# Kernel tuning notes

Measured on AMD Instinct MI355X. Metric: run time of the kernel, lower is better.

The kernel has to match this reference:

```python
import jax, jax.numpy as jnp
import numpy as np

M, K, N = 8192, 4096, 4096


def setup_inputs() -> dict:
    key = jax.random.key(0)
    k1, k2, k3, k4 = jax.random.split(key, 4)
    x = jax.random.normal(k1, (M, K), dtype=jnp.float32)
    # int8 weight buffer (qweight), per-output-channel dequant scales, bf16-style bias
    weight_q = jax.random.randint(k2, (N, K), -128, 128, dtype=jnp.int32).astype(jnp.int8)
    qscales = jax.random.uniform(k3, (N,), dtype=jnp.float32) * 0.01 + 0.005
    bias = jax.random.normal(k4, (N,), dtype=jnp.float32) * 0.01
    return {"x": x, "weight_q": weight_q, "qscales": qscales, "bias": bias}


def reference(x, weight_q, qscales, bias):
    # dynamic per-tensor activation quantization: clampv = max(x)
    clampv = jnp.max(x)
    x8 = jnp.clip(jnp.round(x * (127.0 / clampv)), -128, 127).astype(jnp.int8)
    acc = jax.lax.dot_general(
        x8, weight_q,
        dimension_numbers=(((1,), (1,)), ((), ())),
        preferred_element_type=jnp.int32,
    )
    # fused dequant: (acc*alpha + bias/qscales)*qscales == acc*alpha*qscales + bias
    out = acc.astype(jnp.float32) * (clampv / 127.0) * qscales[None, :] + bias[None, :]
    return out
```

## Files before the change

### kernel.cpp

```cpp
#include <hip/hip_runtime.h>
#include <math.h>

#define MDIM 8192
#define KDIM 4096
#define NDIM 4096

typedef int v4i __attribute__((ext_vector_type(4)));

__device__ __forceinline__ void gload_lds16(const void* g, void* l) {
  __builtin_amdgcn_global_load_lds(
      (const __attribute__((address_space(1))) void*)g,
      (__attribute__((address_space(3))) void*)l,
      16, 0, 0);
}

__global__ void __launch_bounds__(256) kmax(const float* __restrict__ x,
                                            unsigned int* __restrict__ key_out) {
  const int n4 = MDIM * KDIM / 4;
  int tid = blockIdx.x * blockDim.x + threadIdx.x;
  int stride = gridDim.x * blockDim.x;
  float m = -3.4e38f;
  const float4* x4 = (const float4*)x;
  for (int i = tid; i < n4; i += stride) {
    float4 v = x4[i];
    m = fmaxf(m, fmaxf(fmaxf(v.x, v.y), fmaxf(v.z, v.w)));
  }
  #pragma unroll
  for (int off = 32; off > 0; off >>= 1)
    m = fmaxf(m, __shfl_down(m, off, 64));
  __shared__ float sm[4];
  int lane = threadIdx.x & 63, wv = threadIdx.x >> 6;
  if (lane == 0) sm[wv] = m;
  __syncthreads();
  if (threadIdx.x == 0) {
    m = fmaxf(fmaxf(sm[0], sm[1]), fmaxf(sm[2], sm[3]));
    unsigned b = __float_as_uint(m);
    unsigned key = (b & 0x80000000u) ? ~b : (b | 0x80000000u);
    atomicMax(key_out, key);
  }
}

__device__ __forceinline__ float key_to_float(unsigned key) {
  unsigned b = (key & 0x80000000u) ? (key & 0x7FFFFFFFu) : ~key;
  return __uint_as_float(b);
}

__global__ void __launch_bounds__(256) kdetect(const int* __restrict__ w,
                                               unsigned* __restrict__ mode) {
  int ok = 1;
  #pragma unroll
  for (int i = 0; i < 16; ++i) {
    int v = w[threadIdx.x * 16 + i];
    if (v < -128 || v > 127) ok = 0;
  }
  __shared__ int s;
  if (threadIdx.x == 0) s = 1;
  __syncthreads();
  if (!ok) atomicAnd(&s, 0);
  __syncthreads();
  if (threadIdx.x == 0) *mode = (unsigned)s;
}

__global__ void __launch_bounds__(256) kpackw(const int* __restrict__ w,
                                              signed char* __restrict__ w8,
                                              const unsigned* __restrict__ mode) {
  const int n16 = NDIM * KDIM / 16;
  int tid = blockIdx.x * blockDim.x + threadIdx.x;
  int stride = gridDim.x * blockDim.x;
  int4* dst = (int4*)w8;
  if (*mode) {
    const int4* src = (const int4*)w;
    for (int i = tid; i < n16; i += stride) {
      int4 r;
      #pragma unroll
      for (int q = 0; q < 4; ++q) {
        int4 a = src[(size_t)i * 4 + q];
        int packed = (a.x & 255) | ((a.y & 255) << 8) |
                     ((a.z & 255) << 16) | ((a.w & 255) << 24);
        ((int*)&r)[q] = packed;
      }
      dst[i] = r;
    }
  } else {
    const int4* src = (const int4*)w;
    for (int i = tid; i < n16; i += stride) dst[i] = src[i];
  }
}

__device__ __forceinline__ int pack4(float4 v, float s) {
  int q0 = (int)fminf(fmaxf(rintf(v.x * s), -128.f), 127.f);
  int q1 = (int)fminf(fmaxf(rintf(v.y * s), -128.f), 127.f);
  int q2 = (int)fminf(fmaxf(rintf(v.z * s), -128.f), 127.f);
  int q3 = (int)fminf(fmaxf(rintf(v.w * s), -128.f), 127.f);
  return (q0 & 255) | ((q1 & 255) << 8) | ((q2 & 255) << 16) | ((q3 & 255) << 24);
}

__global__ void __launch_bounds__(256) kquant(const float* __restrict__ x,
                                              signed char* __restrict__ x8,
                                              const unsigned* __restrict__ keyp) {
  float s = 127.0f / key_to_float(*keyp);
  const int n16 = MDIM * KDIM / 16;
  int tid = blockIdx.x * blockDim.x + threadIdx.x;
  int stride = gridDim.x * blockDim.x;
  const float4* x4 = (const float4*)x;
  int4* out16 = (int4*)x8;
  for (int i = tid; i < n16; i += stride) {
    const float4* src = x4 + (size_t)i * 4;
    int4 r;
    r.x = pack4(src[0], s);
    r.y = pack4(src[1], s);
    r.z = pack4(src[2], s);
    r.w = pack4(src[3], s);
    out16[i] = r;
  }
}

constexpr int BM = 256, BN = 256, BK = 128;
constexpr int NT = KDIM / BK;

__device__ __forceinline__ v4i mfma_i8(v4i a, v4i b, v4i c) {
  return __builtin_amdgcn_mfma_i32_16x16x64_i8(a, b, c, 0, 0, 0);
}

__global__ void __launch_bounds__(512, 2) kgemm(
    const signed char* __restrict__ A8,
    const signed char* __restrict__ W8,
    const float* __restrict__ qs,
    const float* __restrict__ bias,
    const unsigned* __restrict__ keyp,
    float* __restrict__ out) {
  __shared__ alignas(1024) signed char lds[2][2][BM * BK];

  const int nbn = NDIM / BN;
  const int nwg = (MDIM / BM) * nbn;
  int bid = blockIdx.x;
  int wg = (bid & 7) * (nwg / 8) + (bid >> 3);
  const int brow = (wg / nbn) * BM;
  const int bcol = (wg % nbn) * BN;

  const int tid = threadIdx.x;
  const int lane = tid & 63;
  const int wv = tid >> 6;
  const int wr = wv >> 2, wc = wv & 3;
  const int lhi = lane >> 4, llo = lane & 15;

  const signed char* Abase = A8 + (size_t)brow * KDIM;
  const signed char* Bbase = W8 + (size_t)bcol * KDIM;

  auto stage = [&](int t) {
    const int buf = t & 1;
    const int k0 = t * BK;
    #pragma unroll
    for (int l = 0; l < 4; ++l) {
      int p = l * 512 + tid;
      int row = p >> 3, slot = p & 7;
      int g = slot ^ (row & 7);
      gload_lds16(Abase + (size_t)row * KDIM + k0 + g * 16, &lds[buf][0][p * 16]);
    }
    #pragma unroll
    for (int l = 0; l < 4; ++l) {
      int p = l * 512 + tid;
      int row = p >> 3, slot = p & 7;
      int g = slot ^ (row & 7);
      gload_lds16(Bbase + (size_t)row * KDIM + k0 + g * 16, &lds[buf][1][p * 16]);
    }
  };

  v4i acc[8][4];
  v4i zero = {0, 0, 0, 0};
  #pragma unroll
  for (int i = 0; i < 8; ++i)
    #pragma unroll
    for (int j = 0; j < 4; ++j) acc[i][j] = zero;

  stage(0);
  stage(1);
  asm volatile("s_waitcnt vmcnt(8)" ::: "memory");
  __builtin_amdgcn_s_barrier();
  __builtin_amdgcn_sched_barrier(0);

  for (int t = 0; t < NT; ++t) {
    const int buf = t & 1;
    const signed char* As = lds[buf][0];
    const signed char* Bs = lds[buf][1];

    v4i bfr[4][2];
    #pragma unroll
    for (int ni = 0; ni < 4; ++ni) {
      int row = wc * 64 + ni * 16 + llo;
      #pragma unroll
      for (int ks = 0; ks < 2; ++ks) {
        int slot = (ks * 4 + lhi) ^ (row & 7);
        bfr[ni][ks] = *(const v4i*)&Bs[row * BK + slot * 16];
      }
    }
    #pragma unroll
    for (int ph = 0; ph < 4; ++ph) {
      v4i afr[2][2];
      #pragma unroll
      for (int i = 0; i < 2; ++i) {
        int row = wr * 128 + (2 * ph + i) * 16 + llo;
        #pragma unroll
        for (int ks = 0; ks < 2; ++ks) {
          int slot = (ks * 4 + lhi) ^ (row & 7);
          afr[i][ks] = *(const v4i*)&As[row * BK + slot * 16];
        }
      }
      __builtin_amdgcn_s_setprio(1);
      #pragma unroll
      for (int ni = 0; ni < 4; ++ni) {
        acc[2 * ph][ni]     = mfma_i8(afr[0][0], bfr[ni][0], acc[2 * ph][ni]);
        acc[2 * ph][ni]     = mfma_i8(afr[0][1], bfr[ni][1], acc[2 * ph][ni]);
        acc[2 * ph + 1][ni] = mfma_i8(afr[1][0], bfr[ni][0], acc[2 * ph + 1][ni]);
        acc[2 * ph + 1][ni] = mfma_i8(afr[1][1], bfr[ni][1], acc[2 * ph + 1][ni]);
      }
      __builtin_amdgcn_s_setprio(0);
    }

    __builtin_amdgcn_s_barrier();
    __builtin_amdgcn_sched_barrier(0);
    if (t + 2 < NT) {
      stage(t + 2);
      asm volatile("s_waitcnt vmcnt(8)" ::: "memory");
    } else {
      asm volatile("s_waitcnt vmcnt(0)" ::: "memory");
    }
    __builtin_amdgcn_s_barrier();
    __builtin_amdgcn_sched_barrier(0);
  }

  const float alpha = key_to_float(*keyp) * (1.0f / 127.0f);
  #pragma unroll
  for (int ni = 0; ni < 4; ++ni) {
    int n = bcol + wc * 64 + ni * 16 + llo;
    float sc = qs[n] * alpha;
    float bv = bias[n];
    #pragma unroll
    for (int mi = 0; mi < 8; ++mi) {
      int m0 = brow + wr * 128 + mi * 16 + lhi * 4;
      #pragma unroll
      for (int j = 0; j < 4; ++j)
        out[(size_t)(m0 + j) * NDIM + n] = (float)acc[mi][ni][j] * sc + bv;
    }
  }
}

extern "C" void kernel_launch(void* const* d_in, const int* in_sizes, int n_in,
                              void* d_out, int out_size, void* d_ws, size_t ws_size,
                              hipStream_t stream) {
  const float* x = (const float*)d_in[0];
  const int* wq = (const int*)d_in[1];
  const float* qscales = (const float*)d_in[2];
  const float* bias = (const float*)d_in[3];
  float* out = (float*)d_out;

  unsigned* keyp = (unsigned*)d_ws;
  unsigned* wmode = (unsigned*)d_ws + 1;
  signed char* x8 = (signed char*)d_ws + 256;
  signed char* w8 = x8 + (size_t)MDIM * KDIM;

  hipMemsetAsync(keyp, 0, 4, stream);
  kdetect<<<1, 256, 0, stream>>>(wq, wmode);
  kpackw<<<2048, 256, 0, stream>>>(wq, w8, wmode);
  kmax<<<2048, 256, 0, stream>>>(x, keyp);
  kquant<<<2048, 256, 0, stream>>>(x, x8, keyp);
  kgemm<<<(MDIM / BM) * (NDIM / BN), 512, 0, stream>>>(x8, w8, qscales, bias, keyp, out);
}
```

Baseline: 231.4 us.

## Split GEMM K-step into four phases with half-tile staged prefetch; fold detect into pack

Restructures the int8 GEMM main loop into four MFMA phases per K-tile. Each phase issues a half-tile async global-to-LDS load for the next tiles and waits with a partial vmcnt, so loads and LDS reads interleave more finely with compute. LDS is split into half-tiles with a remapped row layout, and the loop is unrolled by two. Separately, the weight-format detection kernel is merged into the pack kernel, so every block rechecks the format itself and one launch disappears. This adds more barriers per iteration and relies on vmcnt counts and out-of-range prefetch wrapping (t & (NT-1)) being correct.

New measurement: 223.7 us. 1.03x faster.

```diff
diff --git a/kernel.cpp b/kernel.cpp
--- a/kernel.cpp
+++ b/kernel.cpp
@@ -45,30 +45,26 @@
   return __uint_as_float(b);
 }
 
-__global__ void __launch_bounds__(256) kdetect(const int* __restrict__ w,
-                                               unsigned* __restrict__ mode) {
+__global__ void __launch_bounds__(256) kpackw(const int* __restrict__ w,
+                                              signed char* __restrict__ w8) {
+  __shared__ int smode;
   int ok = 1;
   #pragma unroll
   for (int i = 0; i < 16; ++i) {
     int v = w[threadIdx.x * 16 + i];
-    if (v < -128 || v > 127) ok = 0;
-  }
-  __shared__ int s;
-  if (threadIdx.x == 0) s = 1;
+    ok &= (v >= -128) & (v <= 127);
+  }
+  if (threadIdx.x == 0) smode = 1;
   __syncthreads();
-  if (!ok) atomicAnd(&s, 0);
+  if (!ok) atomicAnd(&smode, 0);
   __syncthreads();
-  if (threadIdx.x == 0) *mode = (unsigned)s;
-}
-
-__global__ void __launch_bounds__(256) kpackw(const int* __restrict__ w,
-                                              signed char* __restrict__ w8,
-                                              const unsigned* __restrict__ mode) {
+  const int mode = smode;
+
   const int n16 = NDIM * KDIM / 16;
   int tid = blockIdx.x * blockDim.x + threadIdx.x;
   int stride = gridDim.x * blockDim.x;
   int4* dst = (int4*)w8;
-  if (*mode) {
+  if (mode) {
     const int4* src = (const int4*)w;
     for (int i = tid; i < n16; i += stride) {
       int4 r;
@@ -122,6 +118,13 @@
   return __builtin_amdgcn_mfma_i32_16x16x64_i8(a, b, c, 0, 0, 0);
 }
 
+#define PHASE_END()                                         \
+  do {                                                      \
+    asm volatile("s_waitcnt vmcnt(10)" ::: "memory");       \
+    __builtin_amdgcn_s_barrier();                           \
+    __builtin_amdgcn_sched_barrier(0);                      \
+  } while (0)
+
 __global__ void __launch_bounds__(512, 2) kgemm(
     const signed char* __restrict__ A8,
     const signed char* __restrict__ W8,
@@ -129,7 +132,7 @@
     const float* __restrict__ bias,
     const unsigned* __restrict__ keyp,
     float* __restrict__ out) {
-  __shared__ alignas(1024) signed char lds[2][2][BM * BK];
+  __shared__ alignas(1024) signed char lds[2][2][2][128 * 128];
 
   const int nbn = NDIM / BN;
   const int nwg = (MDIM / BM) * nbn;
@@ -147,23 +150,41 @@
   const signed char* Abase = A8 + (size_t)brow * KDIM;
   const signed char* Bbase = W8 + (size_t)bcol * KDIM;
 
-  auto stage = [&](int t) {
-    const int buf = t & 1;
-    const int k0 = t * BK;
-    #pragma unroll
-    for (int l = 0; l < 4; ++l) {
+  auto stageA = [&](int t, int h) {
+    signed char* dst = &lds[t & 1][0][h][0];
+    const size_t k0 = (size_t)(t & (NT - 1)) * BK;
+    #pragma unroll
+    for (int l = 0; l < 2; ++l) {
       int p = l * 512 + tid;
-      int row = p >> 3, slot = p & 7;
-      int g = slot ^ (row & 7);
-      gload_lds16(Abase + (size_t)row * KDIM + k0 + g * 16, &lds[buf][0][p * 16]);
-    }
-    #pragma unroll
-    for (int l = 0; l < 4; ++l) {
+      int r = p >> 3, s = p & 7;
+      int R = ((r >> 6) << 7) + h * 64 + (r & 63);
+      int g = s ^ (r & 7);
+      gload_lds16(Abase + (size_t)R * KDIM + k0 + g * 16, dst + p * 16);
+    }
+  };
+  auto stageB = [&](int t, int h) {
+    signed char* dst = &lds[t & 1][1][h][0];
+    const size_t k0 = (size_t)(t & (NT - 1)) * BK;
+    #pragma unroll
+    for (int l = 0; l < 2; ++l) {
       int p = l * 512 + tid;
-      int row = p >> 3, slot = p & 7;
-      int g = slot ^ (row & 7);
-      gload_lds16(Bbase + (size_t)row * KDIM + k0 + g * 16, &lds[buf][1][p * 16]);
-    }
+      int r = p >> 3, s = p & 7;
+      int R = ((r >> 5) << 6) + h * 32 + (r & 31);
+      int g = s ^ (r & 7);
+      gload_lds16(Bbase + (size_t)R * KDIM + k0 + g * 16, dst + p * 16);
+    }
+  };
+  auto readA = [&](int par, int mi, int ks) -> v4i {
+    int h = mi >> 2;
+    int r = wr * 64 + (mi & 3) * 16 + llo;
+    int s = (ks * 4 + lhi) ^ (llo & 7);
+    return *(const v4i*)&lds[par][0][h][r * 128 + s * 16];
+  };
+  auto readB = [&](int par, int ni, int ks) -> v4i {
+    int h = ni >> 1;
+    int r = wc * 32 + (ni & 1) * 16 + llo;
+    int s = (ks * 4 + lhi) ^ (llo & 7);
+    return *(const v4i*)&lds[par][1][h][r * 128 + s * 16];
   };
 
   v4i acc[8][4];
@@ -173,61 +194,95 @@
     #pragma unroll
     for (int j = 0; j < 4; ++j) acc[i][j] = zero;
 
-  stage(0);
-  stage(1);
-  asm volatile("s_waitcnt vmcnt(8)" ::: "memory");
+  stageA(0, 0); stageB(0, 0); stageB(0, 1); stageA(0, 1);
+  stageA(1, 0); stageB(1, 0); stageB(1, 1);
+  asm volatile("s_waitcnt vmcnt(6)" ::: "memory");
   __builtin_amdgcn_s_barrier();
   __builtin_amdgcn_sched_barrier(0);
 
+  #pragma unroll 2
   for (int t = 0; t < NT; ++t) {
-    const int buf = t & 1;
-    const signed char* As = lds[buf][0];
-    const signed char* Bs = lds[buf][1];
-
-    v4i bfr[4][2];
-    #pragma unroll
-    for (int ni = 0; ni < 4; ++ni) {
-      int row = wc * 64 + ni * 16 + llo;
-      #pragma unroll
-      for (int ks = 0; ks < 2; ++ks) {
-        int slot = (ks * 4 + lhi) ^ (row & 7);
-        bfr[ni][ks] = *(const v4i*)&Bs[row * BK + slot * 16];
-      }
-    }
-    #pragma unroll
-    for (int ph = 0; ph < 4; ++ph) {
-      v4i afr[2][2];
-      #pragma unroll
-      for (int i = 0; i < 2; ++i) {
-        int row = wr * 128 + (2 * ph + i) * 16 + llo;
-        #pragma unroll
-        for (int ks = 0; ks < 2; ++ks) {
-          int slot = (ks * 4 + lhi) ^ (row & 7);
-          afr[i][ks] = *(const v4i*)&As[row * BK + slot * 16];
-        }
-      }
-      __builtin_amdgcn_s_setprio(1);
-      #pragma unroll
-      for (int ni = 0; ni < 4; ++ni) {
-        acc[2 * ph][ni]     = mfma_i8(afr[0][0], bfr[ni][0], acc[2 * ph][ni]);
-        acc[2 * ph][ni]     = mfma_i8(afr[0][1], bfr[ni][1], acc[2 * ph][ni]);
-        acc[2 * ph + 1][ni] = mfma_i8(afr[1][0], bfr[ni][0], acc[2 * ph + 1][ni]);
-        acc[2 * ph + 1][ni] = mfma_i8(afr[1][1], bfr[ni][1], acc[2 * ph + 1][ni]);
-      }
-      __builtin_amdgcn_s_setprio(0);
-    }
-
+    const int par = t & 1;
+    v4i afr03[4][2], afr47[4][2], bfr01[2][2], bfr23[2][2];
+
+    #pragma unroll
+    for (int mi = 0; mi < 4; ++mi) {
+      afr03[mi][0] = readA(par, mi, 0);
+      afr03[mi][1] = readA(par, mi, 1);
+    }
+    #pragma unroll
+    for (int ni = 0; ni < 2; ++ni) {
+      bfr01[ni][0] = readB(par, ni, 0);
+      bfr01[ni][1] = readB(par, ni, 1);
+    }
+    stageA(t + 1, 1);
     __builtin_amdgcn_s_barrier();
     __builtin_amdgcn_sched_barrier(0);
-    if (t + 2 < NT) {
-      stage(t + 2);
-      asm volatile("s_waitcnt vmcnt(8)" ::: "memory");
-    } else {
-      asm volatile("s_waitcnt vmcnt(0)" ::: "memory");
-    }
+    __builtin_amdgcn_s_setprio(1);
+    #pragma unroll
+    for (int mi = 0; mi < 4; ++mi)
+      #pragma unroll
+      for (int ni = 0; ni < 2; ++ni) {
+        acc[mi][ni] = mfma_i8(afr03[mi][0], bfr01[ni][0], acc[mi][ni]);
+        acc[mi][ni] = mfma_i8(afr03[mi][1], bfr01[ni][1], acc[mi][ni]);
+      }
+    __builtin_amdgcn_s_setprio(0);
+    PHASE_END();
+
+    #pragma unroll
+    for (int ni = 0; ni < 2; ++ni) {
+      bfr23[ni][0] = readB(par, 2 + ni, 0);
+      bfr23[ni][1] = readB(par, 2 + ni, 1);
+    }
+    stageA(t + 2, 0);
     __builtin_amdgcn_s_barrier();
     __builtin_amdgcn_sched_barrier(0);
-  }
+    __builtin_amdgcn_s_setprio(1);
+    #pragma unroll
+    for (int mi = 0; mi < 4; ++mi)
+      #pragma unroll
+      for (int ni = 0; ni < 2; ++ni) {
+        acc[mi][2 + ni] = mfma_i8(afr03[mi][0], bfr23[ni][0], acc[mi][2 + ni]);
+        acc[mi][2 + ni] = mfma_i8(afr03[mi][1], bfr23[ni][1], acc[mi][2 + ni]);
+      }
+    __builtin_amdgcn_s_setprio(0);
+    PHASE_END();
+
+    #pragma unroll
+    for (int mi = 0; mi < 4; ++mi) {
+      afr47[mi][0] = readA(par, 4 + mi, 0);
+      afr47[mi][1] = readA(par, 4 + mi, 1);
+    }
+    stageB(t + 2, 0);
+    __builtin_amdgcn_s_barrier();
+    __builtin_amdgcn_sched_barrier(0);
+    __builtin_amdgcn_s_setprio(1);
+    #pragma unroll
+    for (int mi = 0; mi < 4; ++mi)
+      #pragma unroll
+      for (int ni = 0; ni < 2; ++ni) {
+        acc[4 + mi][ni] = mfma_i8(afr47[mi][0], bfr01[ni][0], acc[4 + mi][ni]);
+        acc[4 + mi][ni] = mfma_i8(afr47[mi][1], bfr01[ni][1], acc[4 + mi][ni]);
+      }
+    __builtin_amdgcn_s_setprio(0);
+    PHASE_END();
+
+    stageB(t + 2, 1);
+    __builtin_amdgcn_s_barrier();
+    __builtin_amdgcn_sched_barrier(0);
+    __builtin_amdgcn_s_setprio(1);
+    #pragma unroll
+    for (int mi = 0; mi < 4; ++mi)
+      #pragma unroll
+      for (int ni = 0; ni < 2; ++ni) {
+        acc[4 + mi][2 + ni] = mfma_i8(afr47[mi][0], bfr23[ni][0], acc[4 + mi][2 + ni]);
+        acc[4 + mi][2 + ni] = mfma_i8(afr47[mi][1], bfr23[ni][1], acc[4 + mi][2 + ni]);
+      }
+    __builtin_amdgcn_s_setprio(0);
+    PHASE_END();
+  }
+
+  asm volatile("s_waitcnt vmcnt(0)" ::: "memory");
 
   const float alpha = key_to_float(*keyp) * (1.0f / 127.0f);
   #pragma unroll
@@ -255,13 +310,11 @@
   float* out = (float*)d_out;
 
   unsigned* keyp = (unsigned*)d_ws;
-  unsigned* wmode = (unsigned*)d_ws + 1;
   signed char* x8 = (signed char*)d_ws + 256;
   signed char* w8 = x8 + (size_t)MDIM * KDIM;
 
   hipMemsetAsync(keyp, 0, 4, stream);
-  kdetect<<<1, 256, 0, stream>>>(wq, wmode);
-  kpackw<<<2048, 256, 0, stream>>>(wq, w8, wmode);
+  kpackw<<<2048, 256, 0, stream>>>(wq, w8);
   kmax<<<2048, 256, 0, stream>>>(x, keyp);
   kquant<<<2048, 256, 0, stream>>>(x, x8, keyp);
   kgemm<<<(MDIM / BM) * (NDIM / BN), 512, 0, stream>>>(x8, w8, qscales, bias, keyp, out);
```
